# Optimization experiments

Hardware: AMD Instinct MI355X
Metric: run time of the kernel (lower is better)

## Reference

```python
import jax, jax.numpy as jnp
import numpy as np

B, C, H, W = 16, 256, 32, 32
NUM_LAYERS = 30
OUT = 16  # sqrt(out_channels)
EPS = 1e-5


def setup_inputs() -> dict:
    key = jax.random.key(0)
    k1, k2, k3 = jax.random.split(key, 3)
    x = jax.random.normal(k1, (B, C, H, W), dtype=jnp.float32)
    # delta_t ~ small positive values (module inits ~N(0.01, 0.005))
    delta_t = jax.random.uniform(k2, (NUM_LAYERS, 1), dtype=jnp.float32) * 0.02
    matrices = jax.random.normal(k3, (NUM_LAYERS, 1, 1, OUT, OUT), dtype=jnp.float32) * 0.1
    gamma = jnp.ones((H * W,), dtype=jnp.float32)   # BatchNorm2d weight, oc = i*i = H*W
    beta = jnp.zeros((H * W,), dtype=jnp.float32)   # BatchNorm2d bias
    return {"x": x, "delta_t": delta_t, "matrices": matrices, "gamma": gamma, "beta": beta}


def _bn_relu6(z, gamma, beta):
    # training-mode BatchNorm2d over channel axis 1 (channels = H*W), then ReLU6
    mean = jnp.mean(z, axis=(0, 2, 3), keepdims=True)
    var = jnp.mean(jnp.square(z - mean), axis=(0, 2, 3), keepdims=True)  # biased var
    zhat = (z - mean) * jax.lax.rsqrt(var + EPS)
    g = gamma.reshape(1, -1, 1, 1)
    b = beta.reshape(1, -1, 1, 1)
    return jnp.clip(zhat * g + b, 0.0, 6.0)


def reference(x, delta_t, matrices, gamma, beta):
    b, c, h, w = x.shape
    hw = h * w
    # feature_reshape: [B,C,H,W] -> [B,HW,C] -> [B,HW,out,out] (inn == out branch)
    x1 = x.reshape(b, c, hw).transpose(0, 2, 1).reshape(b, hw, OUT, OUT)
    dt = jnp.clip(delta_t, 0.0, 6.0)[:, 0]  # relu6(delta_t), shape [L]

    def step(y0, params):
        m, dtl = params  # m: [1,1,out,out] broadcasts elementwise against x1
        dydt = -y0 + _bn_relu6(y0 + m * x1, gamma, beta)
        return y0 + dtl * dydt, None

    y0, _ = jax.lax.scan(step, x1, (matrices, dt))
    # (y0 + x1): [B, HW, out, out] -> view [B,H,W,out*out] -> permute to [B,out*out,H,W]
    y = (y0 + x1).reshape(b, h, w, OUT * OUT).transpose(0, 3, 1, 2)
    return y
```

## Files before the change

### kernel.cpp

```cpp
#include <hip/hip_runtime.h>

#define HW      1024
#define BC      4096
#define NLAYERS 30
#define TPB     256

__global__ __launch_bounds__(TPB) void ode_fused(const float* __restrict__ x,
                                                 const float* __restrict__ delta_t,
                                                 const float* __restrict__ matrices,
                                                 const float* __restrict__ gamma,
                                                 const float* __restrict__ beta,
                                                 float* __restrict__ out) {
    const int p = blockIdx.x;
    const int t = threadIdx.x;

    __shared__ float smat[NLAYERS * 256];
    __shared__ float sdt[NLAYERS];
    __shared__ float red[2][8];

#pragma unroll
    for (int i = 0; i < NLAYERS; ++i)
        smat[i * 256 + t] = matrices[i * 256 + t];
    if (t < NLAYERS)
        sdt[t] = __builtin_amdgcn_fmed3f(delta_t[t], 0.0f, 6.0f);

    float x1[16], y[16];
#pragma unroll
    for (int k = 0; k < 16; ++k)
        x1[k] = x[(size_t)(t + 256 * k) * HW + p];
#pragma unroll
    for (int k = 0; k < 16; ++k) y[k] = x1[k];

    const float gp   = gamma[p];
    const float bp   = beta[p];
    const int   wid  = t >> 6;
    const int   lane = t & 63;

    __syncthreads();

    for (int l = 0; l < NLAYERS; ++l) {
        const float m   = smat[l * 256 + t];
        const float dtl = sdt[l];

        float z[16];
        float s = 0.0f, s2 = 0.0f;
#pragma unroll
        for (int k = 0; k < 16; ++k) {
            const float zz = fmaf(m, x1[k], y[k]);
            z[k] = zz;
            s += zz;
            s2 = fmaf(zz, zz, s2);
        }
#pragma unroll
        for (int mask = 1; mask < 64; mask <<= 1) {
            s  += __shfl_xor(s,  mask, 64);
            s2 += __shfl_xor(s2, mask, 64);
        }
        const int par = l & 1;
        if (lane == 0) { red[par][wid * 2] = s; red[par][wid * 2 + 1] = s2; }
        __syncthreads();
        const float S  = red[par][0] + red[par][2] + red[par][4] + red[par][6];
        const float S2 = red[par][1] + red[par][3] + red[par][5] + red[par][7];

        const float mean = S * (1.0f / 4096.0f);
        const float var  = fmaf(-mean, mean, S2 * (1.0f / 4096.0f));
        const float rstd = rsqrtf(var + 1e-5f);
        const float g    = gp * rstd;
        const float bb   = fmaf(-mean, g, bp);
        const float omdt = 1.0f - dtl;
#pragma unroll
        for (int k = 0; k < 16; ++k) {
            const float a = __builtin_amdgcn_fmed3f(fmaf(z[k], g, bb), 0.0f, 6.0f);
            y[k] = fmaf(dtl, a, omdt * y[k]);
        }
    }

#pragma unroll
    for (int k = 0; k < 16; ++k)
        out[(size_t)(t + 256 * k) * HW + p] = y[k] + x1[k];
}

extern "C" void kernel_launch(void* const* d_in, const int* in_sizes, int n_in,
                              void* d_out, int out_size, void* d_ws, size_t ws_size,
                              hipStream_t stream) {
    const float* x        = (const float*)d_in[0];
    const float* delta_t  = (const float*)d_in[1];
    const float* matrices = (const float*)d_in[2];
    const float* gamma    = (const float*)d_in[3];
    const float* beta     = (const float*)d_in[4];
    float* out = (float*)d_out;

    ode_fused<<<dim3(HW), dim3(TPB), 0, stream>>>(x, delta_t, matrices, gamma, beta, out);
}
```

Baseline: 133.5 us.

## Vectorize ODE layer math with packed float2 ops and swizzle block-to-pixel mapping

Packs the per-thread state into float2 vectors so the FMA, clamp and update math can lower to packed VALU instructions, and splits the sum and sum-of-squares accumulators into independent chains. The block index is also remapped so that consecutive blocks handle pixels spaced 128 apart, which changes how the strided gathers from x and scatters to out spread across channels and caches. The intent is to cut VALU instruction count in the 30-layer loop and improve memory access locality. In exchange, the clamp becomes separate max/min where fmed3 was one instruction, and the swizzle may hurt cache-line sharing between neighbouring blocks.

```diff
diff --git a/kernel.cpp b/kernel.cpp
--- a/kernel.cpp
+++ b/kernel.cpp
@@ -1,4 +1,6 @@
 #include <hip/hip_runtime.h>
+
+typedef float v2f __attribute__((ext_vector_type(2)));
 
 #define HW      1024
 #define BC      4096
@@ -11,12 +13,13 @@
                                                  const float* __restrict__ gamma,
                                                  const float* __restrict__ beta,
                                                  float* __restrict__ out) {
-    const int p = blockIdx.x;
-    const int t = threadIdx.x;
+    const int bid = blockIdx.x;
+    const int p   = ((bid & 7) << 7) | (bid >> 3);
+    const int t   = threadIdx.x;
 
     __shared__ float smat[NLAYERS * 256];
     __shared__ float sdt[NLAYERS];
-    __shared__ float red[2][8];
+    __shared__ v2f   red[2][4];
 
 #pragma unroll
     for (int i = 0; i < NLAYERS; ++i)
@@ -24,12 +27,13 @@
     if (t < NLAYERS)
         sdt[t] = __builtin_amdgcn_fmed3f(delta_t[t], 0.0f, 6.0f);
 
-    float x1[16], y[16];
+    v2f x1[8], y[8];
 #pragma unroll
-    for (int k = 0; k < 16; ++k)
-        x1[k] = x[(size_t)(t + 256 * k) * HW + p];
-#pragma unroll
-    for (int k = 0; k < 16; ++k) y[k] = x1[k];
+    for (int k = 0; k < 8; ++k) {
+        x1[k].x = x[(size_t)(t + 512 * k) * HW + p];
+        x1[k].y = x[(size_t)(t + 512 * k + 256) * HW + p];
+        y[k] = x1[k];
+    }
 
     const float gp   = gamma[p];
     const float bp   = beta[p];
@@ -41,43 +45,58 @@
     for (int l = 0; l < NLAYERS; ++l) {
         const float m   = smat[l * 256 + t];
         const float dtl = sdt[l];
+        const v2f m2 = {m, m};
 
-        float z[16];
-        float s = 0.0f, s2 = 0.0f;
+        v2f z[8];
+        v2f sA = {0.f, 0.f}, sB = {0.f, 0.f};
+        v2f qA = {0.f, 0.f}, qB = {0.f, 0.f};
 #pragma unroll
-        for (int k = 0; k < 16; ++k) {
-            const float zz = fmaf(m, x1[k], y[k]);
-            z[k] = zz;
-            s += zz;
-            s2 = fmaf(zz, zz, s2);
+        for (int k = 0; k < 8; k += 2) {
+            z[k]     = __builtin_elementwise_fma(m2, x1[k], y[k]);
+            z[k + 1] = __builtin_elementwise_fma(m2, x1[k + 1], y[k + 1]);
+            sA += z[k];
+            sB += z[k + 1];
+            qA = __builtin_elementwise_fma(z[k], z[k], qA);
+            qB = __builtin_elementwise_fma(z[k + 1], z[k + 1], qB);
         }
+        const v2f sv = sA + sB;
+        const v2f qv = qA + qB;
+        v2f pr; pr.x = sv.x + sv.y; pr.y = qv.x + qv.y;
+
 #pragma unroll
         for (int mask = 1; mask < 64; mask <<= 1) {
-            s  += __shfl_xor(s,  mask, 64);
-            s2 += __shfl_xor(s2, mask, 64);
+            v2f o;
+            o.x = __shfl_xor(pr.x, mask, 64);
+            o.y = __shfl_xor(pr.y, mask, 64);
+            pr += o;
         }
         const int par = l & 1;
-        if (lane == 0) { red[par][wid * 2] = s; red[par][wid * 2 + 1] = s2; }
+        if (lane == 0) red[par][wid] = pr;
         __syncthreads();
-        const float S  = red[par][0] + red[par][2] + red[par][4] + red[par][6];
-        const float S2 = red[par][1] + red[par][3] + red[par][5] + red[par][7];
+        const v2f tot = red[par][0] + red[par][1] + red[par][2] + red[par][3];
 
-        const float mean = S * (1.0f / 4096.0f);
-        const float var  = fmaf(-mean, mean, S2 * (1.0f / 4096.0f));
+        const float mean = tot.x * (1.0f / 4096.0f);
+        const float var  = fmaf(-mean, mean, tot.y * (1.0f / 4096.0f));
         const float rstd = rsqrtf(var + 1e-5f);
         const float g    = gp * rstd;
         const float bb   = fmaf(-mean, g, bp);
-        const float omdt = 1.0f - dtl;
+        const v2f g2  = {g, g},   b2 = {bb, bb};
+        const v2f dt2 = {dtl, dtl};
+        const v2f z2  = {0.f, 0.f}, s6 = {6.f, 6.f};
 #pragma unroll
-        for (int k = 0; k < 16; ++k) {
-            const float a = __builtin_amdgcn_fmed3f(fmaf(z[k], g, bb), 0.0f, 6.0f);
-            y[k] = fmaf(dtl, a, omdt * y[k]);
+        for (int k = 0; k < 8; ++k) {
+            v2f a = __builtin_elementwise_fma(z[k], g2, b2);
+            a = __builtin_elementwise_max(a, z2);
+            a = __builtin_elementwise_min(a, s6);
+            y[k] = __builtin_elementwise_fma(dt2, a - y[k], y[k]);
         }
     }
 
 #pragma unroll
-    for (int k = 0; k < 16; ++k)
-        out[(size_t)(t + 256 * k) * HW + p] = y[k] + x1[k];
+    for (int k = 0; k < 8; ++k) {
+        out[(size_t)(t + 512 * k) * HW + p]       = y[k].x + x1[k].x;
+        out[(size_t)(t + 512 * k + 256) * HW + p] = y[k].y + x1[k].y;
+    }
 }
 
 extern "C" void kernel_launch(void* const* d_in, const int* in_sizes, int n_in,
```

Result: faster. 121.7 us (-8.8%).
